# Kernel optimization log

Hardware: AMD Instinct MI355X
Metric: run time of the kernel (lower is better)

Reference implementation:

```python
import math
import jax, jax.numpy as jnp
import numpy as np

B, S, T, C, CENC, H, D = 8, 4096, 77, 1280, 2048, 20, 64
STRENGTH = 0.5      # consistency_strength
ALPHA = 0.7         # self_keep_alpha
TOK_P = 0.15        # subject_token_top_p
POS_P = 0.3         # subject_patch_top_p
FIW = 0.5           # feature_injection_weight


def _topk_mask(scores, k):
    # scores: (B, L) -> bool mask (B, L) marking top-k per row
    Bx, L = scores.shape
    idx = jax.lax.top_k(scores, k)[1]
    return jnp.zeros((Bx, L), dtype=bool).at[jnp.arange(Bx)[:, None], idx].set(True)


def _mean_of_others(x):
    # y[i] = mean over j != i of x[j]
    Bx = x.shape[0]
    return (x.sum(axis=0, keepdims=True) - x) / (Bx - 1)


def setup_inputs() -> dict:
    key = jax.random.key(0)
    ks = jax.random.split(key, 7)
    return {
        "hidden_states": jax.random.normal(ks[0], (B, S, C), jnp.float32),
        "encoder_hidden_states": jax.random.normal(ks[1], (B, T, CENC), jnp.float32),
        "Wq": jax.random.normal(ks[2], (C, H * D), jnp.float32) * 0.02,
        "Wk": jax.random.normal(ks[3], (CENC, H * D), jnp.float32) * 0.02,
        "Wv": jax.random.normal(ks[4], (CENC, H * D), jnp.float32) * 0.02,
        "Wo": jax.random.normal(ks[5], (H * D, C), jnp.float32) * 0.02,
        "bo": jnp.zeros((C,), jnp.float32),
    }


def reference(hidden_states, encoder_hidden_states, Wq, Wk, Wv, Wo, bo):
    # project q/k/v and split heads: (B, H, L, D)
    q = (hidden_states @ Wq).reshape(B, S, H, D).transpose(0, 2, 1, 3)
    k = (encoder_hidden_states @ Wk).reshape(B, T, H, D).transpose(0, 2, 1, 3)
    v = (encoder_hidden_states @ Wv).reshape(B, T, H, D).transpose(0, 2, 1, 3)
    scale = 1.0 / math.sqrt(D)

    # first attention pass -> explicit probs (B, H, S, T)
    probs = jax.nn.softmax(jnp.einsum('bhsd,bhtd->bhst', q, k) * scale, axis=-1)

    # subject token mask: aggregate (B,H,S,T) -> (B,T), top-k
    tok_scores = probs.mean(axis=(1, 2))
    k_tok = max(1, int(math.ceil(T * TOK_P)))
    tok_mask = _topk_mask(tok_scores, k_tok)  # (B, T) bool

    # subject position mask: attention mass to subject tokens -> (B,S), top-k
    pos_scores = (probs * tok_mask[:, None, None, :].astype(probs.dtype)).sum(-1).mean(axis=1)
    k_pos = max(1, int(math.ceil(S * POS_P)))
    pos_mask = _topk_mask(pos_scores, k_pos)  # (B, S) bool

    # mask dropout: p = 0.0 -> no-op (deterministic)

    # cross-frame K/V mixing on subject tokens
    tm = tok_mask[:, None, :, None].astype(k.dtype)  # (B,1,T,1)
    def mix(x):
        mixed = ALPHA * x + (1.0 - ALPHA) * _mean_of_others(x)
        return x + STRENGTH * tm * (mixed - x)
    k2, v2 = mix(k), mix(v)

    # second attention pass with mixed K/V
    probs2 = jax.nn.softmax(jnp.einsum('bhsd,bhtd->bhst', q, k2) * scale, axis=-1)
    context = jnp.einsum('bhst,bhtd->bhsd', probs2, v2)

    # patch correspondence injection within subject region
    w = FIW * STRENGTH
    pm = pos_mask[:, None, :, None].astype(context.dtype)  # (B,1,S,1)
    context = context + w * pm * (_mean_of_others(context) - context)

    # merge heads, output projection, residual
    out = context.transpose(0, 2, 1, 3).reshape(B, S, H * D) @ Wo + bo + hidden_states
    return out
```

## Files before the change

kernel.cpp:

```cpp
#include <hip/hip_runtime.h>
#include <math.h>

#define B_    8
#define S_    4096
#define T_    77
#define C_    1280
#define CENC_ 2048
#define H_    20
#define D_    64
#define HD_   1280
#define M1_   (B_*S_)
#define MKV_  (B_*T_)
#define KTOK_ 12
#define KPOS_ 1229
#define SCALE_ 0.125f
#define CMIX_  0.15f
#define CINJ_  (0.25f/7.0f)

typedef __attribute__((ext_vector_type(8))) short bf16x8;
typedef __attribute__((ext_vector_type(4))) float f32x4;

#define AS_G __attribute__((address_space(1)))
#define AS_L __attribute__((address_space(3)))
#define MFMA16 __builtin_amdgcn_mfma_f32_16x16x32_bf16

__device__ inline unsigned short f2bf(float x)
{
    union { float f; unsigned u; } v; v.f = x;
    const unsigned r = v.u + 0x7FFFu + ((v.u >> 16) & 1u);
    return (unsigned short)(r >> 16);
}
__device__ inline float bf2f(unsigned short h)
{
    union { float f; unsigned u; } v; v.u = ((unsigned)h) << 16;
    return v.f;
}

__device__ inline void split_frag(const float* __restrict__ p, bf16x8& hi, bf16x8& lo)
{
    const float4 a = *(const float4*)p;
    const float4 b = *(const float4*)(p + 4);
    float f[8] = {a.x, a.y, a.z, a.w, b.x, b.y, b.z, b.w};
    #pragma unroll
    for (int e = 0; e < 8; ++e) {
        const unsigned short h = f2bf(f[e]);
        hi[e] = (short)h;
        lo[e] = (short)f2bf(f[e] - bf2f(h));
    }
}

__global__ __launch_bounds__(256)
void split_convert_kernel(const float* __restrict__ x, unsigned short* __restrict__ hi,
                          unsigned short* __restrict__ lo)
{
    const size_t i4 = (size_t)blockIdx.x * 256 + threadIdx.x;
    const float4 v = ((const float4*)x)[i4];
    ushort4 h, l;
    h.x = f2bf(v.x); l.x = f2bf(v.x - bf2f(h.x));
    h.y = f2bf(v.y); l.y = f2bf(v.y - bf2f(h.y));
    h.z = f2bf(v.z); l.z = f2bf(v.z - bf2f(h.z));
    h.w = f2bf(v.w); l.w = f2bf(v.w - bf2f(h.w));
    ((ushort4*)hi)[i4] = h;
    ((ushort4*)lo)[i4] = l;
}

__global__ __launch_bounds__(256)
void wsplitT_kernel(const float* __restrict__ W, unsigned short* __restrict__ Thi,
                    unsigned short* __restrict__ Tlo)
{
    __shared__ float tile[32][33];
    const int tx = threadIdx.x & 31, ty = threadIdx.x >> 5;
    const int n0 = blockIdx.x * 32, k0 = blockIdx.y * 32;
    #pragma unroll
    for (int i = 0; i < 4; ++i) {
        const int kk = ty + i * 8;
        tile[kk][tx] = W[(size_t)(k0 + kk) * 1280 + n0 + tx];
    }
    __syncthreads();
    #pragma unroll
    for (int i = 0; i < 4; ++i) {
        const int nn = ty + i * 8;
        const float v = tile[tx][nn];
        const unsigned short h = f2bf(v);
        const size_t oi = (size_t)(n0 + nn) * 1280 + k0 + tx;
        Thi[oi] = h;
        Tlo[oi] = f2bf(v - bf2f(h));
    }
}

__global__ __launch_bounds__(256)
void inject_convert_kernel(const float* __restrict__ ctx, const float* __restrict__ csum,
                           const float* __restrict__ posm, unsigned short* __restrict__ outb)
{
    const size_t i4 = (size_t)blockIdx.x * 256 + threadIdx.x;
    const int row = (int)(i4 / 320);
    const int c4  = (int)(i4 % 320);
    const float cf = posm[row] * CINJ_;
    const float am = 1.0f - 8.0f * cf;
    const float4 c  = ((const float4*)ctx)[i4];
    const float4 cs = ((const float4*)csum)[(size_t)(row & (S_ - 1)) * 320 + c4];
    ushort4 h;
    h.x = f2bf(c.x * am + cf * cs.x);
    h.y = f2bf(c.y * am + cf * cs.y);
    h.z = f2bf(c.z * am + cf * cs.z);
    h.w = f2bf(c.w * am + cf * cs.w);
    ((ushort4*)outb)[i4] = h;
}

__device__ inline void stage_tile(const unsigned short* __restrict__ gsrc,
                                  unsigned short* lds, int tid, int ldK,
                                  int row0, int k0)
{
    #pragma unroll
    for (int c0 = 0; c0 < 512; c0 += 256) {
        const int c = c0 + tid;
        const unsigned short* gp = gsrc + (size_t)(row0 + (c >> 2)) * ldK + k0 + (c & 3) * 8;
        __builtin_amdgcn_global_load_lds((const AS_G void*)gp, (AS_L void*)(lds + (size_t)c * 8),
                                         16, 0, 0);
    }
}

template<bool SPLIT, bool FUSE_OUT>
__global__ __launch_bounds__(256)
void mfma_gemm_kernel(const unsigned short* __restrict__ Ahi, const unsigned short* __restrict__ Alo,
                      const unsigned short* __restrict__ BhiT, const unsigned short* __restrict__ BloT,
                      float* __restrict__ Cout, int K,
                      const float* __restrict__ bias, const float* __restrict__ resid)
{
    __shared__ unsigned short sAhi[128 * 32];
    __shared__ unsigned short sBhi[128 * 32];
    __shared__ unsigned short sAlo[SPLIT ? 128 * 32 : 8];
    __shared__ unsigned short sBlo[SPLIT ? 128 * 32 : 8];

    const int tid  = threadIdx.x;
    const int lane = tid & 63;
    const int wave = tid >> 6;
    const int quad = lane >> 4;
    const int lrow = lane & 15;
    const int wm = (wave & 1) * 64;
    const int wn = (wave >> 1) * 64;

    const int bid = blockIdx.x;
    const int panel = bid / 320;
    const int r = bid % 320;
    const int n0 = (r >> 5) * 128;
    const int m0 = (panel * 32 + (r & 31)) * 128;

    f32x4 acc[4][4] = {};

    for (int k0 = 0; k0 < K; k0 += 32) {
        __syncthreads();
        stage_tile(Ahi,  sAhi, tid, K, m0, k0);
        stage_tile(BhiT, sBhi, tid, K, n0, k0);
        if constexpr (SPLIT) {
            stage_tile(Alo,  sAlo, tid, K, m0, k0);
            stage_tile(BloT, sBlo, tid, K, n0, k0);
        }
        __syncthreads();

        bf16x8 ah[4], bh[4];
        #pragma unroll
        for (int i = 0; i < 4; ++i) {
            ah[i] = *(const bf16x8*)(sAhi + (wm + i * 16 + lrow) * 32 + quad * 8);
            bh[i] = *(const bf16x8*)(sBhi + (wn + i * 16 + lrow) * 32 + quad * 8);
        }
        if constexpr (SPLIT) {
            bf16x8 al[4], bl[4];
            #pragma unroll
            for (int i = 0; i < 4; ++i) {
                al[i] = *(const bf16x8*)(sAlo + (wm + i * 16 + lrow) * 32 + quad * 8);
                bl[i] = *(const bf16x8*)(sBlo + (wn + i * 16 + lrow) * 32 + quad * 8);
            }
            #pragma unroll
            for (int mt = 0; mt < 4; ++mt)
                #pragma unroll
                for (int nt = 0; nt < 4; ++nt) {
                    acc[mt][nt] = MFMA16(ah[mt], bh[nt], acc[mt][nt], 0, 0, 0);
                    acc[mt][nt] = MFMA16(ah[mt], bl[nt], acc[mt][nt], 0, 0, 0);
                    acc[mt][nt] = MFMA16(al[mt], bh[nt], acc[mt][nt], 0, 0, 0);
                }
        } else {
            #pragma unroll
            for (int mt = 0; mt < 4; ++mt)
                #pragma unroll
                for (int nt = 0; nt < 4; ++nt)
                    acc[mt][nt] = MFMA16(ah[mt], bh[nt], acc[mt][nt], 0, 0, 0);
        }
    }

    #pragma unroll
    for (int mt = 0; mt < 4; ++mt) {
        #pragma unroll
        for (int nt = 0; nt < 4; ++nt) {
            const int col = n0 + wn + nt * 16 + lrow;
            #pragma unroll
            for (int r2 = 0; r2 < 4; ++r2) {
                const int row = m0 + wm + mt * 16 + quad * 4 + r2;
                float v = acc[mt][nt][r2];
                if constexpr (FUSE_OUT)
                    v += bias[col] + resid[(size_t)row * 1280 + col];
                Cout[(size_t)row * 1280 + col] = v;
            }
        }
    }
}

__global__ __launch_bounds__(256)
void gemm64_kernel(const float* __restrict__ A,
                   const float* __restrict__ B0, const float* __restrict__ B1,
                   float* __restrict__ C0, float* __restrict__ C1,
                   int M, int N, int K)
{
    const float* Bm = blockIdx.z ? B1 : B0;
    float* Cout = blockIdx.z ? C1 : C0;
    __shared__ float As[16][64];
    __shared__ float Bs[16][64];
    const int tid = threadIdx.x;
    const int n0 = blockIdx.x * 64;
    const int m0 = blockIdx.y * 64;
    const int tx = tid & 15, ty = tid >> 4;
    const int ar = tid >> 2;
    const int ak = (tid & 3) << 2;
    const int bk = tid >> 4;
    const int bn = (tid & 15) << 2;

    float acc[4][4] = {};
    const int arow = m0 + ar;
    const bool avalid = arow < M;
    const float* Ap = A + (size_t)arow * K + ak;
    const float* Bp = Bm + (size_t)bk * N + n0 + bn;

    for (int k0 = 0; k0 < K; k0 += 16) {
        const float4 a = avalid ? *(const float4*)(Ap + k0) : make_float4(0.f,0.f,0.f,0.f);
        const float4 b = *(const float4*)(Bp + (size_t)k0 * N);
        __syncthreads();
        As[ak+0][ar] = a.x; As[ak+1][ar] = a.y; As[ak+2][ar] = a.z; As[ak+3][ar] = a.w;
        *(float4*)&Bs[bk][bn] = b;
        __syncthreads();
        #pragma unroll
        for (int kk = 0; kk < 16; ++kk) {
            const float4 av = *(const float4*)&As[kk][ty*4];
            const float4 bv = *(const float4*)&Bs[kk][tx*4];
            const float arr[4] = {av.x, av.y, av.z, av.w};
            const float brr[4] = {bv.x, bv.y, bv.z, bv.w};
            #pragma unroll
            for (int r = 0; r < 4; ++r)
                #pragma unroll
                for (int c = 0; c < 4; ++c)
                    acc[r][c] = fmaf(arr[r], brr[c], acc[r][c]);
        }
    }
    #pragma unroll
    for (int r = 0; r < 4; ++r) {
        const int row = m0 + ty * 4 + r;
        if (row < M) {
            const float4 cv = make_float4(acc[r][0], acc[r][1], acc[r][2], acc[r][3]);
            *(float4*)(Cout + (size_t)row * N + n0 + tx * 4) = cv;
        }
    }
}

__device__ inline bool first_pair(float va, int ia, float vb, int ib)
{
    return (va > vb) || (va == vb && ia < ib);
}

__device__ inline void bitonic_desc(float* vals, int* idxs, int n, int tid, int nt)
{
    for (int k = 2; k <= n; k <<= 1) {
        for (int j = k >> 1; j > 0; j >>= 1) {
            __syncthreads();
            for (int i = tid; i < n; i += nt) {
                const int l = i ^ j;
                if (l > i) {
                    const float vi = vals[i], vl = vals[l];
                    const int   ii = idxs[i], il = idxs[l];
                    const bool up = (i & k) == 0;
                    const bool sw = up ? first_pair(vl, il, vi, ii)
                                       : first_pair(vi, ii, vl, il);
                    if (sw) { vals[i] = vl; vals[l] = vi; idxs[i] = il; idxs[l] = ii; }
                }
            }
        }
    }
    __syncthreads();
}

__global__ __launch_bounds__(256)
void pass_a_kernel(const float* __restrict__ q, const float* __restrict__ kbuf,
                   float* __restrict__ tokp)
{
    __shared__ unsigned short khi[80 * 64];
    __shared__ unsigned short klo[80 * 64];
    __shared__ float wsum[4][80];
    const int g = blockIdx.x;
    const int b = g / 320;
    const int rem = g % 320;
    const int h = rem >> 4;
    const int chunk = rem & 15;
    const int tid = threadIdx.x;

    for (int i = tid; i < 80 * 16; i += 256) {
        const int t = i >> 4, j = i & 15;
        float4 v = make_float4(0.f, 0.f, 0.f, 0.f);
        if (t < T_) v = *(const float4*)(kbuf + (size_t)(b * T_ + t) * HD_ + h * D_ + 4 * j);
        ushort4 hh, ll;
        hh.x = f2bf(v.x); ll.x = f2bf(v.x - bf2f(hh.x));
        hh.y = f2bf(v.y); ll.y = f2bf(v.y - bf2f(hh.y));
        hh.z = f2bf(v.z); ll.z = f2bf(v.z - bf2f(hh.z));
        hh.w = f2bf(v.w); ll.w = f2bf(v.w - bf2f(hh.w));
        const int byt = t * 128 + ((8 * j) ^ ((t & 7) << 4));
        *(ushort4*)((char*)khi + byt) = hh;
        *(ushort4*)((char*)klo + byt) = ll;
    }
    __syncthreads();

    const int wid = tid >> 6, lane = tid & 63;
    const int lrow = lane & 15, quad = lane >> 4;

    f32x4 tokacc[5] = {};
    for (int st = 0; st < 4; ++st) {
        const int s = chunk * 256 + wid * 64 + st * 16 + lrow;
        const float* qp = q + (size_t)(b * S_ + s) * HD_ + h * D_;
        bf16x8 qhi[2], qlo[2];
        #pragma unroll
        for (int ks = 0; ks < 2; ++ks)
            split_frag(qp + ks * 32 + quad * 8, qhi[ks], qlo[ks]);

        f32x4 acc[5] = {};
        #pragma unroll
        for (int nt = 0; nt < 5; ++nt) {
            #pragma unroll
            for (int ks = 0; ks < 2; ++ks) {
                const int krow = nt * 16 + lrow;
                const int byt = krow * 128 + ((64 * ks + 16 * quad) ^ ((krow & 7) << 4));
                const bf16x8 kh = *(const bf16x8*)((const char*)khi + byt);
                const bf16x8 kl = *(const bf16x8*)((const char*)klo + byt);
                acc[nt] = MFMA16(kh, qhi[ks], acc[nt], 0, 0, 0);
                acc[nt] = MFMA16(kh, qlo[ks], acc[nt], 0, 0, 0);
                acc[nt] = MFMA16(kl, qhi[ks], acc[nt], 0, 0, 0);
                acc[nt] = MFMA16(kl, qlo[ks], acc[nt], 0, 0, 0);
            }
        }
        float m = -1e30f;
        #pragma unroll
        for (int nt = 0; nt < 5; ++nt)
            #pragma unroll
            for (int r = 0; r < 4; ++r) {
                const int t = nt * 16 + quad * 4 + r;
                const float l = (t < T_) ? acc[nt][r] * SCALE_ : -1e30f;
                acc[nt][r] = l;
                m = fmaxf(m, l);
            }
        m = fmaxf(m, __shfl_xor(m, 16, 64));
        m = fmaxf(m, __shfl_xor(m, 32, 64));
        float Lp = 0.f;
        #pragma unroll
        for (int nt = 0; nt < 5; ++nt)
            #pragma unroll
            for (int r = 0; r < 4; ++r) {
                const float e = __expf(acc[nt][r] - m);
                acc[nt][r] = e;
                Lp += e;
            }
        float L = Lp + __shfl_xor(Lp, 16, 64);
        L += __shfl_xor(L, 32, 64);
        const float invL = 1.0f / L;
        #pragma unroll
        for (int nt = 0; nt < 5; ++nt)
            #pragma unroll
            for (int r = 0; r < 4; ++r)
                tokacc[nt][r] = fmaf(acc[nt][r], invL, tokacc[nt][r]);
    }
    #pragma unroll
    for (int nt = 0; nt < 5; ++nt)
        #pragma unroll
        for (int r = 0; r < 4; ++r) {
            float v = tokacc[nt][r];
            v += __shfl_xor(v, 1, 64);
            v += __shfl_xor(v, 2, 64);
            v += __shfl_xor(v, 4, 64);
            v += __shfl_xor(v, 8, 64);
            if (lrow == 0) wsum[wid][nt * 16 + quad * 4 + r] = v;
        }
    __syncthreads();
    for (int t = tid; t < T_; t += 256)
        tokp[(size_t)g * T_ + t] = (wsum[0][t] + wsum[1][t]) + (wsum[2][t] + wsum[3][t]);
}

__global__ __launch_bounds__(128)
void topk_tok_kernel(const float* __restrict__ tokp, float* __restrict__ tokm)
{
    __shared__ float vals[128];
    __shared__ int idxs[128];
    const int b = blockIdx.x, tid = threadIdx.x;
    float v = -1e30f;
    if (tid < T_) {
        float sm = 0.f;
        for (int j = 0; j < 320; ++j) sm += tokp[(size_t)(b * 320 + j) * T_ + tid];
        v = sm;
    }
    vals[tid] = v; idxs[tid] = tid;
    bitonic_desc(vals, idxs, 128, tid, 128);
    if (tid < T_) tokm[b * T_ + tid] = 0.f;
    __syncthreads();
    if (tid < KTOK_) tokm[b * T_ + idxs[tid]] = 1.0f;
}

__global__ __launch_bounds__(256)
void mix_kernel(const float* __restrict__ kbuf, const float* __restrict__ vbuf,
                const float* __restrict__ tokm,
                float* __restrict__ kd, float* __restrict__ v2)
{
    const int i = blockIdx.x * 256 + threadIdx.x;
    const int t = i / HD_;
    float ks = 0.f, vs = 0.f;
    #pragma unroll
    for (int b = 0; b < B_; ++b) {
        ks += kbuf[(size_t)b * T_ * HD_ + i];
        vs += vbuf[(size_t)b * T_ * HD_ + i];
    }
    #pragma unroll
    for (int b = 0; b < B_; ++b) {
        const size_t gi = (size_t)b * T_ * HD_ + i;
        const float msk = tokm[b * T_ + t];
        const float kx = kbuf[gi], vx = vbuf[gi];
        kd[gi] = CMIX_ * msk * ((ks - 8.f * kx) * (1.0f / 7.0f));
        v2[gi] = vx + CMIX_ * msk * ((vs - 8.f * vx) * (1.0f / 7.0f));
    }
}

__global__ __launch_bounds__(256)
void pass_bc_kernel(const float* __restrict__ q, const float* __restrict__ kbuf,
                    const float* __restrict__ kd, const float* __restrict__ v2,
                    const float* __restrict__ tokm,
                    float* __restrict__ posp, float* __restrict__ ctx)
{
    __shared__ unsigned short khi[80 * 64];
    __shared__ unsigned short klo[80 * 64];
    __shared__ unsigned short kdh[80 * 64];
    __shared__ unsigned short vThi[64 * 88];
    __shared__ unsigned short vTlo[64 * 88];
    __shared__ unsigned short vguard[128];
    __shared__ unsigned short Pbuf[4][2][16 * 40];
    __shared__ float smaskf[80];

    const int g = blockIdx.x;
    const int b = g / 320;
    const int rem = g % 320;
    const int h = rem >> 4;
    const int chunk = rem & 15;
    const int tid = threadIdx.x;

    for (int i = tid; i < 80 * 16; i += 256) {
        const int t = i >> 4, j = i & 15;
        float4 vk = make_float4(0.f, 0.f, 0.f, 0.f);
        float4 vd = make_float4(0.f, 0.f, 0.f, 0.f);
        if (t < T_) {
            const size_t gi = (size_t)(b * T_ + t) * HD_ + h * D_ + 4 * j;
            vk = *(const float4*)(kbuf + gi);
            vd = *(const float4*)(kd + gi);
        }
        ushort4 hh, ll, dd;
        hh.x = f2bf(vk.x); ll.x = f2bf(vk.x - bf2f(hh.x)); dd.x = f2bf(vd.x);
        hh.y = f2bf(vk.y); ll.y = f2bf(vk.y - bf2f(hh.y)); dd.y = f2bf(vd.y);
        hh.z = f2bf(vk.z); ll.z = f2bf(vk.z - bf2f(hh.z)); dd.z = f2bf(vd.z);
        hh.w = f2bf(vk.w); ll.w = f2bf(vk.w - bf2f(hh.w)); dd.w = f2bf(vd.w);
        const int byt = t * 128 + ((8 * j) ^ ((t & 7) << 4));
        *(ushort4*)((char*)khi + byt) = hh;
        *(ushort4*)((char*)klo + byt) = ll;
        *(ushort4*)((char*)kdh + byt) = dd;
    }
    for (int i = tid; i < 64 * 22; i += 256) {
        const int d = i / 22, jg = i - d * 22;
        float vv[4];
        #pragma unroll
        for (int r = 0; r < 4; ++r) {
            const int t = 4 * jg + r;
            vv[r] = (t < T_) ? v2[(size_t)(b * T_ + t) * HD_ + h * D_ + d] : 0.f;
        }
        ushort4 hh, ll;
        hh.x = f2bf(vv[0]); ll.x = f2bf(vv[0] - bf2f(hh.x));
        hh.y = f2bf(vv[1]); ll.y = f2bf(vv[1] - bf2f(hh.y));
        hh.z = f2bf(vv[2]); ll.z = f2bf(vv[2] - bf2f(hh.z));
        hh.w = f2bf(vv[3]); ll.w = f2bf(vv[3] - bf2f(hh.w));
        const int byt = d * 176 + 8 * jg;
        *(ushort4*)((char*)vThi + byt) = hh;
        *(ushort4*)((char*)vTlo + byt) = ll;
    }
    for (int t = tid; t < 80; t += 256) smaskf[t] = (t < T_) ? tokm[b * T_ + t] : 0.f;
    for (int i = tid; i < 128; i += 256) vguard[i] = 0;
    __syncthreads();

    const int wid = tid >> 6, lane = tid & 63;
    const int lrow = lane & 15, quad = lane >> 4;
    unsigned short* Ph = &Pbuf[wid][0][0];
    unsigned short* Pl = &Pbuf[wid][1][0];

    float smv[5][4];
    #pragma unroll
    for (int nt = 0; nt < 5; ++nt)
        #pragma unroll
        for (int r = 0; r < 4; ++r)
            smv[nt][r] = smaskf[nt * 16 + quad * 4 + r];

    for (int st = 0; st < 4; ++st) {
        const int s = chunk * 256 + wid * 64 + st * 16 + lrow;
        const float* qp = q + (size_t)(b * S_ + s) * HD_ + h * D_;
        bf16x8 qhi[2], qlo[2];
        #pragma unroll
        for (int ks = 0; ks < 2; ++ks)
            split_frag(qp + ks * 32 + quad * 8, qhi[ks], qlo[ks]);

        f32x4 acc1[5] = {}, accd[5] = {};
        #pragma unroll
        for (int nt = 0; nt < 5; ++nt) {
            #pragma unroll
            for (int ks = 0; ks < 2; ++ks) {
                const int krow = nt * 16 + lrow;
                const int byt = krow * 128 + ((64 * ks + 16 * quad) ^ ((krow & 7) << 4));
                const bf16x8 kh = *(const bf16x8*)((const char*)khi + byt);
                const bf16x8 kl = *(const bf16x8*)((const char*)klo + byt);
                const bf16x8 kdv = *(const bf16x8*)((const char*)kdh + byt);
                acc1[nt] = MFMA16(kh, qhi[ks], acc1[nt], 0, 0, 0);
                acc1[nt] = MFMA16(kh, qlo[ks], acc1[nt], 0, 0, 0);
                acc1[nt] = MFMA16(kl, qhi[ks], acc1[nt], 0, 0, 0);
                acc1[nt] = MFMA16(kl, qlo[ks], acc1[nt], 0, 0, 0);
                accd[nt] = MFMA16(kdv, qhi[ks], accd[nt], 0, 0, 0);
            }
        }

        float m1 = -1e30f, m2 = -1e30f;
        f32x4 l2v[5];
        #pragma unroll
        for (int nt = 0; nt < 5; ++nt)
            #pragma unroll
            for (int r = 0; r < 4; ++r) {
                const int t = nt * 16 + quad * 4 + r;
                const bool valid = t < T_;
                const float l1 = valid ? acc1[nt][r] * SCALE_ : -1e30f;
                const float l2 = valid ? l1 + accd[nt][r] * SCALE_ : -1e30f;
                acc1[nt][r] = l1;
                l2v[nt][r] = l2;
                m1 = fmaxf(m1, l1);
                m2 = fmaxf(m2, l2);
            }
        m1 = fmaxf(m1, __shfl_xor(m1, 16, 64));
        m1 = fmaxf(m1, __shfl_xor(m1, 32, 64));
        m2 = fmaxf(m2, __shfl_xor(m2, 16, 64));
        m2 = fmaxf(m2, __shfl_xor(m2, 32, 64));
        float L1p = 0.f, Smp = 0.f, L2p = 0.f;
        #pragma unroll
        for (int nt = 0; nt < 5; ++nt)
            #pragma unroll
            for (int r = 0; r < 4; ++r) {
                const float e1 = __expf(acc1[nt][r] - m1);
                L1p += e1;
                Smp = fmaf(e1, smv[nt][r], Smp);
                const float e2 = __expf(l2v[nt][r] - m2);
                l2v[nt][r] = e2;
                L2p += e2;
            }
        float L1 = L1p + __shfl_xor(L1p, 16, 64); L1 += __shfl_xor(L1, 32, 64);
        float Sm = Smp + __shfl_xor(Smp, 16, 64); Sm += __shfl_xor(Sm, 32, 64);
        float L2 = L2p + __shfl_xor(L2p, 16, 64); L2 += __shfl_xor(L2, 32, 64);
        if (quad == 0) posp[(size_t)(b * H_ + h) * S_ + s] = Sm / L1;
        const float invL2 = 1.0f / L2;
        #pragma unroll
        for (int nt = 0; nt < 5; ++nt)
            #pragma unroll
            for (int r = 0; r < 4; ++r)
                l2v[nt][r] *= invL2;

        f32x4 pv[4] = {};
        #pragma unroll
        for (int ks = 0; ks < 3; ++ks) {
            asm volatile("s_waitcnt lgkmcnt(0)" ::: "memory");
            __builtin_amdgcn_sched_barrier(0);
            #pragma unroll
            for (int half = 0; half < 2; ++half) {
                const int nt = 2 * ks + half;
                ushort4 ph = {0, 0, 0, 0}, plw = {0, 0, 0, 0};
                if (nt < 5) {
                    ph.x = f2bf(l2v[nt][0]); plw.x = f2bf(l2v[nt][0] - bf2f(ph.x));
                    ph.y = f2bf(l2v[nt][1]); plw.y = f2bf(l2v[nt][1] - bf2f(ph.y));
                    ph.z = f2bf(l2v[nt][2]); plw.z = f2bf(l2v[nt][2] - bf2f(ph.z));
                    ph.w = f2bf(l2v[nt][3]); plw.w = f2bf(l2v[nt][3] - bf2f(ph.w));
                }
                const int pb = lrow * 80 + 32 * half + 8 * quad;
                *(ushort4*)((char*)Ph + pb) = ph;
                *(ushort4*)((char*)Pl + pb) = plw;
            }
            asm volatile("s_waitcnt lgkmcnt(0)" ::: "memory");
            __builtin_amdgcn_sched_barrier(0);
            const bf16x8 pH = *(const bf16x8*)((const char*)Ph + lrow * 80 + quad * 16);
            const bf16x8 pL = *(const bf16x8*)((const char*)Pl + lrow * 80 + quad * 16);
            #pragma unroll
            for (int mt = 0; mt < 4; ++mt) {
                const int vb = (mt * 16 + lrow) * 176 + 64 * ks + 16 * quad;
                const bf16x8 vH = *(const bf16x8*)((const char*)vThi + vb);
                const bf16x8 vL = *(const bf16x8*)((const char*)vTlo + vb);
                pv[mt] = MFMA16(vH, pH, pv[mt], 0, 0, 0);
                pv[mt] = MFMA16(vH, pL, pv[mt], 0, 0, 0);
                pv[mt] = MFMA16(vL, pH, pv[mt], 0, 0, 0);
            }
        }
        float* cp = ctx + (size_t)(b * S_ + s) * HD_ + h * D_;
        #pragma unroll
        for (int mt = 0; mt < 4; ++mt) {
            const float4 o = make_float4(pv[mt][0], pv[mt][1], pv[mt][2], pv[mt][3]);
            *(float4*)(cp + mt * 16 + quad * 4) = o;
        }
    }
}

__global__ __launch_bounds__(1024)
void topk_pos_kernel(const float* __restrict__ posp, float* __restrict__ posm)
{
    __shared__ float vals[S_];
    __shared__ int idxs[S_];
    const int b = blockIdx.x, tid = threadIdx.x;
    for (int s = tid; s < S_; s += 1024) {
        float sm = 0.f;
        for (int h = 0; h < H_; ++h) sm += posp[(size_t)(b * H_ + h) * S_ + s];
        vals[s] = sm; idxs[s] = s;
    }
    bitonic_desc(vals, idxs, S_, tid, 1024);
    for (int s = tid; s < S_; s += 1024) posm[b * S_ + s] = 0.f;
    __syncthreads();
    for (int i = tid; i < KPOS_; i += 1024) posm[b * S_ + idxs[i]] = 1.0f;
}

__global__ __launch_bounds__(256)
void ctxsum_kernel(const float* __restrict__ ctx, float* __restrict__ csum)
{
    const size_t i = (size_t)blockIdx.x * 256 + threadIdx.x;
    const float4* c = (const float4*)ctx;
    float4 a = c[i];
    #pragma unroll
    for (int b = 1; b < B_; ++b) {
        const float4 x = c[(size_t)b * (S_ * HD_ / 4) + i];
        a.x += x.x; a.y += x.y; a.z += x.z; a.w += x.w;
    }
    ((float4*)csum)[i] = a;
}

extern "C" void kernel_launch(void* const* d_in, const int* in_sizes, int n_in,
                              void* d_out, int out_size, void* d_ws, size_t ws_size,
                              hipStream_t stream)
{
    const float* hidden = (const float*)d_in[0];
    const float* enc    = (const float*)d_in[1];
    const float* Wq     = (const float*)d_in[2];
    const float* Wk     = (const float*)d_in[3];
    const float* Wv     = (const float*)d_in[4];
    const float* Wo     = (const float*)d_in[5];
    const float* bo     = (const float*)d_in[6];
    float* out = (float*)d_out;

    char* w = (char*)d_ws;
    float* q    = (float*)w; w += (size_t)M1_ * HD_ * 4;
    float* ctx  = (float*)w; w += (size_t)M1_ * HD_ * 4;
    float* kbuf = (float*)w; w += (size_t)B_ * T_ * HD_ * 4;
    float* vbuf = (float*)w; w += (size_t)B_ * T_ * HD_ * 4;
    float* kd   = (float*)w; w += (size_t)B_ * T_ * HD_ * 4;
    float* v2   = (float*)w; w += (size_t)B_ * T_ * HD_ * 4;
    float* csum = (float*)w; w += (size_t)S_ * HD_ * 4;
    float* tokp = (float*)w; w += (size_t)2560 * T_ * 4;
    float* posp = (float*)w; w += (size_t)B_ * H_ * S_ * 4;
    float* tokm = (float*)w; w += (size_t)B_ * T_ * 4;
    float* posm = (float*)w; w += (size_t)B_ * S_ * 4;
    unsigned short* Ahi   = (unsigned short*)w; w += (size_t)M1_ * HD_ * 2;
    unsigned short* Alo   = (unsigned short*)w; w += (size_t)M1_ * HD_ * 2;
    unsigned short* ctxb  = (unsigned short*)w; w += (size_t)M1_ * HD_ * 2;
    unsigned short* WqhiT = (unsigned short*)w; w += (size_t)C_ * HD_ * 2;
    unsigned short* WqloT = (unsigned short*)w; w += (size_t)C_ * HD_ * 2;
    unsigned short* WohiT = (unsigned short*)w; w += (size_t)HD_ * C_ * 2;
    unsigned short* WoloT = (unsigned short*)w; w += (size_t)HD_ * C_ * 2;
    (void)ws_size; (void)in_sizes; (void)n_in; (void)out_size;

    split_convert_kernel<<<M1_ * HD_ / 4 / 256, 256, 0, stream>>>(hidden, Ahi, Alo);
    wsplitT_kernel<<<dim3(40, 40), 256, 0, stream>>>(Wq, WqhiT, WqloT);
    wsplitT_kernel<<<dim3(40, 40), 256, 0, stream>>>(Wo, WohiT, WoloT);
    mfma_gemm_kernel<true, false><<<2560, 256, 0, stream>>>(
        Ahi, Alo, WqhiT, WqloT, q, C_, nullptr, nullptr);
    gemm64_kernel<<<dim3(20, 10, 2), 256, 0, stream>>>(
        enc, Wk, Wv, kbuf, vbuf, MKV_, HD_, CENC_);
    pass_a_kernel<<<2560, 256, 0, stream>>>(q, kbuf, tokp);
    topk_tok_kernel<<<8, 128, 0, stream>>>(tokp, tokm);
    mix_kernel<<<385, 256, 0, stream>>>(kbuf, vbuf, tokm, kd, v2);
    pass_bc_kernel<<<2560, 256, 0, stream>>>(q, kbuf, kd, v2, tokm, posp, ctx);
    topk_pos_kernel<<<8, 1024, 0, stream>>>(posp, posm);
    ctxsum_kernel<<<S_ * HD_ / 4 / 256, 256, 0, stream>>>(ctx, csum);
    inject_convert_kernel<<<M1_ * HD_ / 4 / 256, 256, 0, stream>>>(ctx, csum, posm, ctxb);
    mfma_gemm_kernel<false, true><<<2560, 256, 0, stream>>>(
        ctxb, nullptr, WohiT, nullptr, out, HD_, bo, hidden);
}
```

Baseline: 1.546 ms.

## Replace MFMA GEMMs with 256x256 double-buffered, 8-wave pipelined GEMM kernel

Replaces the 128x128 single-buffered MFMA GEMM with a 512-thread kernel that computes 256x256 output tiles. It double-buffers LDS and interleaves global-to-LDS staging with MFMA phases, using raw barriers, waitcnt and setprio. The split-precision Q projection is expressed as three concatenated K segments (hi*hi, hi*lo, lo*hi) in a single K loop, and blocks are swizzled across XCDs. The aim is to raise MFMA utilisation and hide load latency. In exchange the kernel needs much more LDS and registers and relies on fragile hand-tuned waitcnt counts.

```diff
diff --git a/kernel.cpp b/kernel.cpp
--- a/kernel.cpp
+++ b/kernel.cpp
@@ -16,6 +16,7 @@
 #define SCALE_ 0.125f
 #define CMIX_  0.15f
 #define CINJ_  (0.25f/7.0f)
+#define SEGT_  20
 
 typedef __attribute__((ext_vector_type(8))) short bf16x8;
 typedef __attribute__((ext_vector_type(4))) float f32x4;
@@ -23,6 +24,10 @@
 #define AS_G __attribute__((address_space(1)))
 #define AS_L __attribute__((address_space(3)))
 #define MFMA16 __builtin_amdgcn_mfma_f32_16x16x32_bf16
+#define SBAR() asm volatile("s_barrier" ::: "memory")
+#define VM8 asm volatile("s_waitcnt vmcnt(8)" ::: "memory")
+#define VM0 asm volatile("s_waitcnt vmcnt(0)" ::: "memory")
+#define NOP ((void)0)
 
 __device__ inline unsigned short f2bf(float x)
 {
@@ -107,97 +112,132 @@
     ((ushort4*)outb)[i4] = h;
 }
 
-__device__ inline void stage_tile(const unsigned short* __restrict__ gsrc,
-                                  unsigned short* lds, int tid, int ldK,
-                                  int row0, int k0)
-{
-    #pragma unroll
-    for (int c0 = 0; c0 < 512; c0 += 256) {
-        const int c = c0 + tid;
-        const unsigned short* gp = gsrc + (size_t)(row0 + (c >> 2)) * ldK + k0 + (c & 3) * 8;
-        __builtin_amdgcn_global_load_lds((const AS_G void*)gp, (AS_L void*)(lds + (size_t)c * 8),
-                                         16, 0, 0);
-    }
-}
-
-template<bool SPLIT, bool FUSE_OUT>
-__global__ __launch_bounds__(256)
-void mfma_gemm_kernel(const unsigned short* __restrict__ Ahi, const unsigned short* __restrict__ Alo,
-                      const unsigned short* __restrict__ BhiT, const unsigned short* __restrict__ BloT,
-                      float* __restrict__ Cout, int K,
-                      const float* __restrict__ bias, const float* __restrict__ resid)
-{
-    __shared__ unsigned short sAhi[128 * 32];
-    __shared__ unsigned short sBhi[128 * 32];
-    __shared__ unsigned short sAlo[SPLIT ? 128 * 32 : 8];
-    __shared__ unsigned short sBlo[SPLIT ? 128 * 32 : 8];
+#define PHASE(BUF, KS, MH, RB, STG, VM)                                         \
+    {                                                                           \
+        const unsigned short* SAp = sA[BUF];                                    \
+        _Pragma("unroll")                                                       \
+        for (int j = 0; j < 4; ++j)                                             \
+            aF[j] = *(const bf16x8*)(SAp + ((((KS)*4+quad)*256) + wr*128 + (MH)*64 + j*16 + lrow)*8); \
+        if (RB) {                                                               \
+            const unsigned short* SBp = sB[BUF];                                \
+            _Pragma("unroll")                                                   \
+            for (int g = 0; g < 4; ++g)                                         \
+                bF[g] = *(const bf16x8*)(SBp + ((((KS)*4+quad)*256) + wc*64 + g*16 + lrow)*8); \
+        }                                                                       \
+        STG;                                                                    \
+        SBAR();                                                                 \
+        asm volatile("s_waitcnt lgkmcnt(0)" ::: "memory");                      \
+        __builtin_amdgcn_sched_barrier(0);                                      \
+        __builtin_amdgcn_s_setprio(1);                                          \
+        _Pragma("unroll")                                                       \
+        for (int j = 0; j < 4; ++j)                                             \
+            _Pragma("unroll")                                                   \
+            for (int g = 0; g < 4; ++g)                                         \
+                acc[(MH)*4+j][g] = MFMA16(aF[j], bF[g], acc[(MH)*4+j][g], 0, 0, 0); \
+        __builtin_amdgcn_s_setprio(0);                                          \
+        VM;                                                                     \
+        SBAR();                                                                 \
+    }
+
+template<bool FUSE>
+__global__ __launch_bounds__(512, 2)
+void gemm8p_kernel(const unsigned short* __restrict__ A0, const unsigned short* __restrict__ A1,
+                   const unsigned short* __restrict__ A2,
+                   const unsigned short* __restrict__ B0, const unsigned short* __restrict__ B1,
+                   const unsigned short* __restrict__ B2,
+                   float* __restrict__ Cout, int NTILES,
+                   const float* __restrict__ bias, const float* __restrict__ resid)
+{
+    __shared__ unsigned short sA[2][16384];
+    __shared__ unsigned short sB[2][16384];
 
     const int tid  = threadIdx.x;
     const int lane = tid & 63;
-    const int wave = tid >> 6;
+    const int wid  = tid >> 6;
     const int quad = lane >> 4;
     const int lrow = lane & 15;
-    const int wm = (wave & 1) * 64;
-    const int wn = (wave >> 1) * 64;
-
-    const int bid = blockIdx.x;
-    const int panel = bid / 320;
-    const int r = bid % 320;
-    const int n0 = (r >> 5) * 128;
-    const int m0 = (panel * 32 + (r & 31)) * 128;
-
-    f32x4 acc[4][4] = {};
-
-    for (int k0 = 0; k0 < K; k0 += 32) {
-        __syncthreads();
-        stage_tile(Ahi,  sAhi, tid, K, m0, k0);
-        stage_tile(BhiT, sBhi, tid, K, n0, k0);
-        if constexpr (SPLIT) {
-            stage_tile(Alo,  sAlo, tid, K, m0, k0);
-            stage_tile(BloT, sBlo, tid, K, n0, k0);
-        }
-        __syncthreads();
-
-        bf16x8 ah[4], bh[4];
-        #pragma unroll
-        for (int i = 0; i < 4; ++i) {
-            ah[i] = *(const bf16x8*)(sAhi + (wm + i * 16 + lrow) * 32 + quad * 8);
-            bh[i] = *(const bf16x8*)(sBhi + (wn + i * 16 + lrow) * 32 + quad * 8);
-        }
-        if constexpr (SPLIT) {
-            bf16x8 al[4], bl[4];
-            #pragma unroll
-            for (int i = 0; i < 4; ++i) {
-                al[i] = *(const bf16x8*)(sAlo + (wm + i * 16 + lrow) * 32 + quad * 8);
-                bl[i] = *(const bf16x8*)(sBlo + (wn + i * 16 + lrow) * 32 + quad * 8);
-            }
-            #pragma unroll
-            for (int mt = 0; mt < 4; ++mt)
-                #pragma unroll
-                for (int nt = 0; nt < 4; ++nt) {
-                    acc[mt][nt] = MFMA16(ah[mt], bh[nt], acc[mt][nt], 0, 0, 0);
-                    acc[mt][nt] = MFMA16(ah[mt], bl[nt], acc[mt][nt], 0, 0, 0);
-                    acc[mt][nt] = MFMA16(al[mt], bh[nt], acc[mt][nt], 0, 0, 0);
-                }
-        } else {
-            #pragma unroll
-            for (int mt = 0; mt < 4; ++mt)
-                #pragma unroll
-                for (int nt = 0; nt < 4; ++nt)
-                    acc[mt][nt] = MFMA16(ah[mt], bh[nt], acc[mt][nt], 0, 0, 0);
-        }
-    }
-
-    #pragma unroll
-    for (int mt = 0; mt < 4; ++mt) {
-        #pragma unroll
-        for (int nt = 0; nt < 4; ++nt) {
-            const int col = n0 + wn + nt * 16 + lrow;
+    const int wr = wid >> 2;
+    const int wc = wid & 3;
+
+    const int nwg = gridDim.x;
+    const int cpx = nwg >> 3;
+    int sw = ((int)blockIdx.x & 7) * cpx + ((int)blockIdx.x >> 3);
+    const int m0 = (sw & 127) * 256;
+    const int n0 = (sw >> 7) * 256;
+
+    int voff[2], cdst[2];
+    #pragma unroll
+    for (int j = 0; j < 2; ++j) {
+        const int c = tid + j * 512;
+        voff[j] = (c & 255) * 1280 + (c >> 8) * 8;
+        cdst[j] = c * 8;
+    }
+
+    auto stageA = [&](int t, int ks) {
+        const int seg = t / SEGT_;
+        const int kt  = t - seg * SEGT_;
+        const unsigned short* Ab = (seg == 0) ? A0 : (seg == 1) ? A1 : A2;
+        const size_t base = (size_t)m0 * 1280 + kt * 64 + ks * 32;
+        unsigned short* reg = &sA[t & 1][ks * 8192];
+        #pragma unroll
+        for (int j = 0; j < 2; ++j)
+            __builtin_amdgcn_global_load_lds((const AS_G void*)(Ab + base + voff[j]),
+                                             (AS_L void*)(reg + cdst[j]), 16, 0, 0);
+    };
+    auto stageB = [&](int t, int ks) {
+        const int seg = t / SEGT_;
+        const int kt  = t - seg * SEGT_;
+        const unsigned short* Bb = (seg == 0) ? B0 : (seg == 1) ? B1 : B2;
+        const size_t base = (size_t)n0 * 1280 + kt * 64 + ks * 32;
+        unsigned short* reg = &sB[t & 1][ks * 8192];
+        #pragma unroll
+        for (int j = 0; j < 2; ++j)
+            __builtin_amdgcn_global_load_lds((const AS_G void*)(Bb + base + voff[j]),
+                                             (AS_L void*)(reg + cdst[j]), 16, 0, 0);
+    };
+
+    f32x4 acc[8][4] = {};
+    bf16x8 aF[4], bF[4];
+
+    const int NI = NTILES >> 1;
+
+    stageA(0, 0); stageB(0, 0); stageA(0, 1); stageB(0, 1); stageA(1, 0); stageB(1, 0);
+    VM8;
+    SBAR();
+
+    for (int it = 0; it < NI - 1; ++it) {
+        const int t0 = 2 * it, t1 = 2 * it + 1;
+        PHASE(0, 0, 0, true,  stageA(t1, 1),     NOP);
+        PHASE(0, 0, 1, false, stageB(t1, 1),     VM8);
+        PHASE(0, 1, 0, true,  stageA(t0 + 2, 0), NOP);
+        PHASE(0, 1, 1, false, stageB(t0 + 2, 0), VM8);
+        PHASE(1, 0, 0, true,  stageA(t0 + 2, 1), NOP);
+        PHASE(1, 0, 1, false, stageB(t0 + 2, 1), VM8);
+        PHASE(1, 1, 0, true,  stageA(t1 + 2, 0), NOP);
+        PHASE(1, 1, 1, false, stageB(t1 + 2, 0), VM8);
+    }
+    {
+        const int t1 = NTILES - 1;
+        PHASE(0, 0, 0, true,  stageA(t1, 1), NOP);
+        PHASE(0, 0, 1, false, stageB(t1, 1), VM0);
+        PHASE(0, 1, 0, true,  NOP, NOP);
+        PHASE(0, 1, 1, false, NOP, NOP);
+        PHASE(1, 0, 0, true,  NOP, NOP);
+        PHASE(1, 0, 1, false, NOP, NOP);
+        PHASE(1, 1, 0, true,  NOP, NOP);
+        PHASE(1, 1, 1, false, NOP, NOP);
+    }
+
+    #pragma unroll
+    for (int f = 0; f < 8; ++f) {
+        #pragma unroll
+        for (int g = 0; g < 4; ++g) {
+            const int col = n0 + wc * 64 + g * 16 + lrow;
             #pragma unroll
             for (int r2 = 0; r2 < 4; ++r2) {
-                const int row = m0 + wm + mt * 16 + quad * 4 + r2;
-                float v = acc[mt][nt][r2];
-                if constexpr (FUSE_OUT)
+                const int row = m0 + wr * 128 + f * 16 + quad * 4 + r2;
+                float v = acc[f][g][r2];
+                if constexpr (FUSE)
                     v += bias[col] + resid[(size_t)row * 1280 + col];
                 Cout[(size_t)row * 1280 + col] = v;
             }
@@ -682,8 +722,8 @@
     split_convert_kernel<<<M1_ * HD_ / 4 / 256, 256, 0, stream>>>(hidden, Ahi, Alo);
     wsplitT_kernel<<<dim3(40, 40), 256, 0, stream>>>(Wq, WqhiT, WqloT);
     wsplitT_kernel<<<dim3(40, 40), 256, 0, stream>>>(Wo, WohiT, WoloT);
-    mfma_gemm_kernel<true, false><<<2560, 256, 0, stream>>>(
-        Ahi, Alo, WqhiT, WqloT, q, C_, nullptr, nullptr);
+    gemm8p_kernel<false><<<640, 512, 0, stream>>>(
+        Ahi, Ahi, Alo, WqhiT, WqloT, WqhiT, q, 60, nullptr, nullptr);
     gemm64_kernel<<<dim3(20, 10, 2), 256, 0, stream>>>(
         enc, Wk, Wv, kbuf, vbuf, MKV_, HD_, CENC_);
     pass_a_kernel<<<2560, 256, 0, stream>>>(q, kbuf, tokp);
@@ -693,6 +733,6 @@
     topk_pos_kernel<<<8, 1024, 0, stream>>>(posp, posm);
     ctxsum_kernel<<<S_ * HD_ / 4 / 256, 256, 0, stream>>>(ctx, csum);
     inject_convert_kernel<<<M1_ * HD_ / 4 / 256, 256, 0, stream>>>(ctx, csum, posm, ctxb);
-    mfma_gemm_kernel<false, true><<<2560, 256, 0, stream>>>(
-        ctxb, nullptr, WohiT, nullptr, out, HD_, bo, hidden);
-}
+    gemm8p_kernel<true><<<640, 512, 0, stream>>>(
+        ctxb, ctxb, ctxb, WohiT, WohiT, WohiT, out, 20, bo, hidden);
+}
```

After: 1.779 ms. 15.0% more time.
